# Kernel optimization log

Measured on AMD Instinct MI355X. Metric: run time of the kernel, lower is better.

Reference implementation:

```python
import jax, jax.numpy as jnp
import numpy as np

T, N, F_IN, H1, H2, F_OUT = 48, 4096, 64, 64, 32, 64

def setup_inputs() -> dict:
    key = jax.random.key(0)
    ks = jax.random.split(key, 14)
    sc = 0.05
    x = jax.random.normal(ks[0], (T, N, F_IN), jnp.float32)
    adj = jax.random.uniform(ks[1], (N, N), jnp.float32) / N  # roughly row-normalized dense adjacency
    fc_w = jax.random.normal(ks[2], (F_IN, H1), jnp.float32) * sc
    fc_b = jnp.zeros((H1,), jnp.float32)
    Wz = jax.random.normal(ks[3], (H1, F_OUT), jnp.float32) * sc
    Wr = jax.random.normal(ks[4], (H1, F_OUT), jnp.float32) * sc
    Wh = jax.random.normal(ks[5], (H1, F_OUT), jnp.float32) * sc
    Lz = jax.random.normal(ks[6], (2 * F_OUT, F_OUT), jnp.float32) * sc
    Lr = jax.random.normal(ks[7], (2 * F_OUT, F_OUT), jnp.float32) * sc
    Lh = jax.random.normal(ks[8], (2 * F_OUT, F_OUT), jnp.float32) * sc
    bz = jnp.zeros((F_OUT,), jnp.float32)
    br = jnp.zeros((F_OUT,), jnp.float32)
    bh = jnp.zeros((F_OUT,), jnp.float32)
    return {"x": x, "adj": adj, "fc_w": fc_w, "fc_b": fc_b,
            "Wz": Wz, "Wr": Wr, "Wh": Wh,
            "Lz": Lz, "Lr": Lr, "Lh": Lh,
            "bz": bz, "br": br, "bh": bh}

def reference(x, adj, fc_w, fc_b, Wz, Wr, Wh, Lz, Lr, Lh, bz, br, bh):
    # relu(fc(x)) followed by relu(unsqueeze) == single relu
    xh = jax.nn.relu(x @ fc_w + fc_b)          # [T, N, H1]
    h0 = jnp.zeros((N, F_OUT), x.dtype)

    def step(h, xi):
        # TGCN cell: dense graph conv A @ (X W) feeding GRU-style gates
        az = adj @ (xi @ Wz)                   # [N, F_OUT]
        ar = adj @ (xi @ Wr)
        ah = adj @ (xi @ Wh)
        z = jax.nn.sigmoid(jnp.concatenate([az, h], axis=-1) @ Lz + bz)
        r = jax.nn.sigmoid(jnp.concatenate([ar, h], axis=-1) @ Lr + br)
        h_tilde = jnp.tanh(jnp.concatenate([ah, h * r], axis=-1) @ Lh + bh)
        h_new = z * h + (1.0 - z) * h_tilde
        return h_new, None

    h, _ = jax.lax.scan(step, h0, xh)
    return h[None]                              # [1, N, F_OUT]
```

## Files before the change

kernel.cpp:

```cpp
#include <hip/hip_runtime.h>

typedef unsigned short u16;
typedef unsigned char u8;
typedef short s16x8 __attribute__((ext_vector_type(8)));
typedef unsigned short u16x4 __attribute__((ext_vector_type(4)));
typedef float f32x4 __attribute__((ext_vector_type(4)));
typedef int i32x4 __attribute__((ext_vector_type(4)));
typedef int i32x8 __attribute__((ext_vector_type(8)));

#define AS1 __attribute__((address_space(1)))
#define AS3 __attribute__((address_space(3)))

__device__ __forceinline__ void g2l16(const void* g, void* l) {
  __builtin_amdgcn_global_load_lds((const AS1 void*)g, (AS3 void*)l, 16, 0, 0);
}

__device__ __forceinline__ float b2f(u16 u) {
  union { unsigned int i; float f; } x; x.i = ((unsigned int)u) << 16; return x.f;
}
__device__ __forceinline__ u16 f2b(float f) {
  unsigned int u = __builtin_bit_cast(unsigned int, f);
  return (u16)((u + 0x7fffu + ((u >> 16) & 1u)) >> 16);
}
__device__ __forceinline__ u8 f2e4m3(float v) {
  int p = __builtin_amdgcn_cvt_pk_fp8_f32(v, 0.f, 0, false);
  return (u8)(p & 0xff);
}
__device__ __forceinline__ float sigm(float x) { return 1.f / (1.f + __expf(-x)); }
__device__ __forceinline__ float tanh_f(float x) { return 2.f / (1.f + __expf(-2.f * x)) - 1.f; }


__global__ __launch_bounds__(256) void kpre(
    const float* __restrict__ a, u8* __restrict__ ab,
    const float* __restrict__ fcw, const float* __restrict__ fcb,
    const float* __restrict__ x, u8* __restrict__ xht,
    const float* __restrict__ Wz, const float* __restrict__ Wr, const float* __restrict__ Wh,
    const float* __restrict__ Lz, const float* __restrict__ Lr, const float* __restrict__ Lh,
    u16* __restrict__ wct, u16* __restrict__ lbt) {
  int b = blockIdx.x, tid = threadIdx.x;
  if (b < 4096) {
    size_t idx = (size_t)b * 256 + tid;
    const float4* src = (const float4*)a;
    unsigned int* dst = (unsigned int*)ab;
#pragma unroll
    for (int k = 0; k < 4; ++k) {
      float4 v = src[idx + (size_t)k * 1048576];
      unsigned int p = __builtin_amdgcn_cvt_pk_fp8_f32(v.x * 4096.f, v.y * 4096.f, 0, false);
      p = __builtin_amdgcn_cvt_pk_fp8_f32(v.z * 4096.f, v.w * 4096.f, p, true);
      dst[idx + (size_t)k * 1048576] = p;
    }
    return;
  }
  if (b < 4144) {
    int idx = (b - 4096) * 256 + tid;
    int c_cat = idx >> 6, hh = idx & 63;
    int g = c_cat >> 6, c = c_cat & 63;
    const float* W = (g == 0) ? Wz : (g == 1) ? Wr : Wh;
    const float* L = (g == 0) ? Lz : (g == 1) ? Lr : Lh;
    float acc = 0.f;
    for (int m = 0; m < 64; ++m) acc += W[hh * 64 + m] * L[m * 64 + c];
    wct[c_cat * 64 + hh] = f2b(acc);
    return;
  }
  if (b < 4147) {
    int g = b - 4144;
    const float* L = (g == 0) ? Lz : (g == 1) ? Lr : Lh;
    for (int i = 0; i < 16; ++i) {
      int idx = tid * 16 + i; int c = idx >> 6, hh = idx & 63;
      lbt[g * 4096 + c * 64 + hh] = f2b(L[(64 + hh) * 64 + c]);
    }
    return;
  }
  int kb = b - 4147;
  int t = kb >> 5, n0 = (kb & 31) * 128;
  __shared__ __align__(16) u16 xs[128 * 72];
  __shared__ __align__(16) u16 fw[64 * 72];
  __shared__ __align__(16) u8 xh8[64 * 128];
  __shared__ float fb[64];
  int w = tid >> 6, l = tid & 63;
#pragma unroll
  for (int i = 0; i < 16; ++i) {
    int idx = tid + i * 256;
    int h = idx & 63, f = idx >> 6;
    fw[h * 72 + f] = f2b(fcw[f * 64 + h]);
  }
  const float4* xg = (const float4*)(x + ((size_t)t * 4096 + n0) * 64);
#pragma unroll
  for (int i = 0; i < 8; ++i) {
    int f = tid + i * 256;
    float4 v = xg[f];
    u16x4 p; p[0] = f2b(v.x); p[1] = f2b(v.y); p[2] = f2b(v.z); p[3] = f2b(v.w);
    *(u16x4*)&xs[(f >> 4) * 72 + (f & 15) * 4] = p;
  }
  if (tid < 64) fb[tid] = fcb[tid];
  __syncthreads();

  int lm = l & 15, q = l >> 4;
  f32x4 acc[4][2];
#pragma unroll
  for (int i = 0; i < 4; ++i)
#pragma unroll
    for (int j = 0; j < 2; ++j)
#pragma unroll
      for (int r = 0; r < 4; ++r) acc[i][j][r] = 0.f;
#pragma unroll
  for (int s = 0; s < 2; ++s) {
    s16x8 af[4], bf[2];
#pragma unroll
    for (int i = 0; i < 4; ++i) af[i] = *(const s16x8*)&fw[(16 * i + lm) * 72 + 32 * s + q * 8];
#pragma unroll
    for (int j = 0; j < 2; ++j) bf[j] = *(const s16x8*)&xs[(32 * w + 16 * j + lm) * 72 + 32 * s + q * 8];
#pragma unroll
    for (int i = 0; i < 4; ++i)
#pragma unroll
      for (int j = 0; j < 2; ++j)
        acc[i][j] = __builtin_amdgcn_mfma_f32_16x16x32_bf16(af[i], bf[j], acc[i][j], 0, 0, 0);
  }
#pragma unroll
  for (int i = 0; i < 4; ++i)
#pragma unroll
    for (int j = 0; j < 2; ++j) {
      int node = 32 * w + 16 * j + lm;
      int h0 = 16 * i + q * 4;
#pragma unroll
      for (int r = 0; r < 4; ++r) {
        float v = acc[i][j][r] + fb[h0 + r];
        xh8[(h0 + r) * 128 + node] = f2e4m3(v > 0.f ? v : 0.f);
      }
    }
  __syncthreads();
  {
    int h = tid >> 2, seg = tid & 3;
    u8* dst = xht + (size_t)(t * 64 + h) * 4096 + n0 + seg * 32;
    const u8* src = &xh8[h * 128 + seg * 32];
    *(i32x4*)dst = *(const i32x4*)src;
    *(i32x4*)(dst + 16) = *(const i32x4*)(src + 16);
  }
}

__global__ __launch_bounds__(256, 2) void k2(
    const u8* __restrict__ A, const u8* __restrict__ B, u16* __restrict__ M) {
  __shared__ __align__(16) u8 sh[49152];
  int tid = threadIdx.x, w = tid >> 6, l = tid & 63;
  int nt = blockIdx.x, mt = blockIdx.y;
  const u8* Ab = A + (size_t)mt * 128 * 4096;
  const u8* Bb = B + (size_t)nt * 192 * 4096;
  int lm = l & 15, q = l >> 4;
  int wm = w >> 1, wn = w & 1;
  int srow = l >> 3, scol = l & 7;
  f32x4 acc[4][6];
#pragma unroll
  for (int i = 0; i < 4; ++i)
#pragma unroll
    for (int j = 0; j < 6; ++j)
#pragma unroll
      for (int r = 0; r < 4; ++r) acc[i][j][r] = 0.f;

#define STAGE_B(bsel, kk)                                                     \
  do {                                                                        \
    _Pragma("unroll") for (int j = 0; j < 6; ++j) {                           \
      int r0 = 48 * w + 8 * j;                                                \
      int row = r0 + srow;                                                    \
      int c = (scol - row) & 7;                                               \
      g2l16(Bb + (size_t)row * 4096 + (kk) + c * 16,                          \
            sh + (bsel) * 24576 + r0 * 128);                                  \
    }                                                                         \
  } while (0)

  STAGE_B(0, 0);
  __syncthreads();

  for (int it = 0; it < 32; ++it) {
    int k0b = it * 128;
    int cur = it & 1;
    i32x8 a8[4];
#pragma unroll
    for (int i = 0; i < 4; ++i) {
      int ra = 64 * wm + 16 * i + lm;
      a8[i] = *(const i32x8*)(Ab + (size_t)ra * 4096 + k0b + q * 32);
    }
    if (it < 31) STAGE_B(cur ^ 1, k0b + 128);
    const u8* Bs = sh + cur * 24576;
#pragma unroll
    for (int j = 0; j < 6; ++j) {
      int rb = 96 * wn + 16 * j + lm;
      int q0 = (2 * q + rb) & 7, q1 = (2 * q + 1 + rb) & 7;
      i32x4 lo = *(const i32x4*)&Bs[rb * 128 + q0 * 16];
      i32x4 hi = *(const i32x4*)&Bs[rb * 128 + q1 * 16];
      i32x8 b8 = __builtin_shufflevector(lo, hi, 0, 1, 2, 3, 4, 5, 6, 7);
#pragma unroll
      for (int i = 0; i < 4; ++i)
        acc[i][j] = __builtin_amdgcn_mfma_scale_f32_16x16x128_f8f6f4(
            a8[i], b8, acc[i][j], 0, 0, 0, 127, 0, 127);
    }
    __syncthreads();
  }
#undef STAGE_B

  u16* tb = (u16*)sh;
  const float sc = 1.f / 4096.f;
#pragma unroll
  for (int p = 0; p < 2; ++p) {
    if (p) __syncthreads();
    if (wm == p) {
#pragma unroll
      for (int i = 0; i < 4; ++i)
#pragma unroll
        for (int j = 0; j < 6; ++j)
#pragma unroll
          for (int r = 0; r < 4; ++r)
            tb[(16 * i + 4 * q + r) * 200 + 96 * wn + 16 * j + lm] = f2b(acc[i][j][r] * sc);
    }
    __syncthreads();
    int row = tid >> 2, seg = tid & 3;
    u16* dst = M + (size_t)(mt * 128 + p * 64 + row) * 3072 + nt * 192 + seg * 48;
    const u16* src = &tb[row * 200 + seg * 48];
#pragma unroll
    for (int v = 0; v < 6; ++v)
      *(i32x4*)(dst + 8 * v) = *(const i32x4*)(src + 8 * v);
  }
}

__global__ __launch_bounds__(256) void k3(
    const u16* __restrict__ M, const u16* __restrict__ wct, const u16* __restrict__ lbt,
    const float* __restrict__ bz, const float* __restrict__ br, const float* __restrict__ bh,
    float* __restrict__ out) {
  __shared__ __align__(16) u16 hhi[16 * 72], hlo[16 * 72];
  __shared__ __align__(16) u16 rhi[16 * 72], rlo[16 * 72];
  int tid = threadIdx.x, w = tid >> 6, l = tid & 63;
  int nb0 = blockIdx.x * 16;
  int lm = l & 15, q = l >> 4;
  int cb = 16 * w + q * 4;
  s16x8 afw[3][2], afl[3][2];
#pragma unroll
  for (int g = 0; g < 3; ++g)
#pragma unroll
    for (int s = 0; s < 2; ++s) {
      afw[g][s] = *(const s16x8*)&wct[(size_t)(g * 64 + 16 * w + lm) * 64 + 32 * s + q * 8];
      afl[g][s] = *(const s16x8*)&lbt[(size_t)(g * 64 + 16 * w + lm) * 64 + 32 * s + q * 8];
    }
  for (int i = tid; i < 16 * 72; i += 256) { hhi[i] = 0; hlo[i] = 0; }
  f32x4 bzv, brv, bhv, hv;
#pragma unroll
  for (int r = 0; r < 4; ++r) {
    bzv[r] = bz[cb + r]; brv[r] = br[cb + r]; bhv[r] = bh[cb + r]; hv[r] = 0.f;
  }
  __syncthreads();

  const u16* Mrow = M + (size_t)(nb0 + lm) * 3072;
  s16x8 Mn[2];
  Mn[0] = *(const s16x8*)&Mrow[q * 8];
  Mn[1] = *(const s16x8*)&Mrow[32 + q * 8];

  for (int t = 0; t < 48; ++t) {
    s16x8 Mc[2] = {Mn[0], Mn[1]};
    if (t < 47) {
      Mn[0] = *(const s16x8*)&Mrow[(t + 1) * 64 + q * 8];
      Mn[1] = *(const s16x8*)&Mrow[(t + 1) * 64 + 32 + q * 8];
    }
    f32x4 uzw, uzh, urw, urh;
#pragma unroll
    for (int r = 0; r < 4; ++r) { uzw[r] = 0.f; uzh[r] = 0.f; urw[r] = 0.f; urh[r] = 0.f; }
#pragma unroll
    for (int s = 0; s < 2; ++s) {
      s16x8 hh = *(const s16x8*)&hhi[lm * 72 + 32 * s + q * 8];
      s16x8 hl = *(const s16x8*)&hlo[lm * 72 + 32 * s + q * 8];
      uzw = __builtin_amdgcn_mfma_f32_16x16x32_bf16(afw[0][s], Mc[s], uzw, 0, 0, 0);
      uzh = __builtin_amdgcn_mfma_f32_16x16x32_bf16(afl[0][s], hh, uzh, 0, 0, 0);
      uzh = __builtin_amdgcn_mfma_f32_16x16x32_bf16(afl[0][s], hl, uzh, 0, 0, 0);
      urw = __builtin_amdgcn_mfma_f32_16x16x32_bf16(afw[1][s], Mc[s], urw, 0, 0, 0);
      urh = __builtin_amdgcn_mfma_f32_16x16x32_bf16(afl[1][s], hh, urh, 0, 0, 0);
      urh = __builtin_amdgcn_mfma_f32_16x16x32_bf16(afl[1][s], hl, urh, 0, 0, 0);
    }
    f32x4 zv, rv;
#pragma unroll
    for (int r = 0; r < 4; ++r) {
      zv[r] = sigm(uzw[r] + uzh[r] + bzv[r]);
      rv[r] = sigm(urw[r] + urh[r] + brv[r]);
    }
    {
      u16x4 phi, plo;
#pragma unroll
      for (int r = 0; r < 4; ++r) {
        float p = hv[r] * rv[r];
        u16 hi = f2b(p); phi[r] = hi; plo[r] = f2b(p - b2f(hi));
      }
      *(u16x4*)&rhi[lm * 72 + cb] = phi;
      *(u16x4*)&rlo[lm * 72 + cb] = plo;
    }
    __syncthreads();
    f32x4 uhw, uhh;
#pragma unroll
    for (int r = 0; r < 4; ++r) { uhw[r] = 0.f; uhh[r] = 0.f; }
#pragma unroll
    for (int s = 0; s < 2; ++s) {
      s16x8 rh = *(const s16x8*)&rhi[lm * 72 + 32 * s + q * 8];
      s16x8 rl = *(const s16x8*)&rlo[lm * 72 + 32 * s + q * 8];
      uhw = __builtin_amdgcn_mfma_f32_16x16x32_bf16(afw[2][s], Mc[s], uhw, 0, 0, 0);
      uhh = __builtin_amdgcn_mfma_f32_16x16x32_bf16(afl[2][s], rh, uhh, 0, 0, 0);
      uhh = __builtin_amdgcn_mfma_f32_16x16x32_bf16(afl[2][s], rl, uhh, 0, 0, 0);
    }
    {
      u16x4 phi, plo;
#pragma unroll
      for (int r = 0; r < 4; ++r) {
        float th = tanh_f(uhw[r] + uhh[r] + bhv[r]);
        float hn = zv[r] * hv[r] + (1.f - zv[r]) * th;
        hv[r] = hn;
        u16 hi = f2b(hn); phi[r] = hi; plo[r] = f2b(hn - b2f(hi));
      }
      *(u16x4*)&hhi[lm * 72 + cb] = phi;
      *(u16x4*)&hlo[lm * 72 + cb] = plo;
    }
    __syncthreads();
  }
#pragma unroll
  for (int r = 0; r < 4; ++r)
    out[(size_t)(nb0 + lm) * 64 + cb + r] = hv[r];
}

extern "C" void kernel_launch(void* const* d_in, const int* in_sizes, int n_in,
                              void* d_out, int out_size, void* d_ws, size_t ws_size,
                              hipStream_t stream) {
  const float* x   = (const float*)d_in[0];
  const float* adj = (const float*)d_in[1];
  const float* fcw = (const float*)d_in[2];
  const float* fcb = (const float*)d_in[3];
  const float* Wz  = (const float*)d_in[4];
  const float* Wr  = (const float*)d_in[5];
  const float* Wh  = (const float*)d_in[6];
  const float* Lz  = (const float*)d_in[7];
  const float* Lr  = (const float*)d_in[8];
  const float* Lh  = (const float*)d_in[9];
  const float* bz  = (const float*)d_in[10];
  const float* br  = (const float*)d_in[11];
  const float* bh  = (const float*)d_in[12];
  char* ws = (char*)d_ws;
  u8*  xht  = (u8*)(ws);
  u8*  adj8 = (u8*)(ws + (size_t)12582912);
  u16* Mm   = (u16*)(ws + (size_t)29360128);
  u16* wct  = (u16*)(ws + (size_t)54525952);
  u16* lbt  = (u16*)(ws + (size_t)54550528);
  float* outp = (float*)d_out;

  hipLaunchKernelGGL(kpre, dim3(5683), dim3(256), 0, stream,
                     adj, adj8, fcw, fcb, x, xht, Wz, Wr, Wh, Lz, Lr, Lh, wct, lbt);
  hipLaunchKernelGGL(k2, dim3(16, 32), dim3(256), 0, stream, adj8, xht, Mm);
  hipLaunchKernelGGL(k3, dim3(256), dim3(256), 0, stream, Mm, wct, lbt, bz, br, bh, outp);
}
```

Baseline: 285.9 us.

## Stage A tiles through LDS alongside B in double-buffered k2 GEMM

The A operand of the fp8 MFMA GEMM was read straight from global memory into registers each iteration. It is now loaded asynchronously into LDS with the same swizzled global_load_lds scheme used for B, double-buffered, and read back from LDS with conflict-avoiding offsets. The prefetch of the next stage is also issued before the current compute. LDS per block grows from 48KB to 80KB and the occupancy hint of 2 blocks per CU is dropped, which may reduce concurrency.

Result: faster. 259.3 us (-9.3%).

```diff
diff --git a/kernel.cpp b/kernel.cpp
--- a/kernel.cpp
+++ b/kernel.cpp
@@ -138,9 +138,9 @@
   }
 }
 
-__global__ __launch_bounds__(256, 2) void k2(
+__global__ __launch_bounds__(256) void k2(
     const u8* __restrict__ A, const u8* __restrict__ B, u16* __restrict__ M) {
-  __shared__ __align__(16) u8 sh[49152];
+  __shared__ __align__(16) u8 sh[81920];
   int tid = threadIdx.x, w = tid >> 6, l = tid & 63;
   int nt = blockIdx.x, mt = blockIdx.y;
   const u8* Ab = A + (size_t)mt * 128 * 4096;
@@ -156,38 +156,49 @@
 #pragma unroll
       for (int r = 0; r < 4; ++r) acc[i][j][r] = 0.f;
 
-#define STAGE_B(bsel, kk)                                                     \
+#define STAGE(bsel, kk)                                                       \
   do {                                                                        \
-    _Pragma("unroll") for (int j = 0; j < 6; ++j) {                           \
+    u8* As_ = sh + (bsel) * 40960;                                            \
+    u8* Bs_ = As_ + 16384;                                                    \
+    _Pragma("unroll") for (int j = 0; j < 4; ++j) {      \
+      int r0 = 32 * w + 8 * j;                                                \
+      int row = r0 + srow;                                                    \
+      int c = (scol - row) & 7;                                               \
+      g2l16(Ab + (size_t)row * 4096 + (kk) + c * 16, As_ + r0 * 128);         \
+    }                                                                         \
+    _Pragma("unroll") for (int j = 0; j < 6; ++j) {      \
       int r0 = 48 * w + 8 * j;                                                \
       int row = r0 + srow;                                                    \
       int c = (scol - row) & 7;                                               \
-      g2l16(Bb + (size_t)row * 4096 + (kk) + c * 16,                          \
-            sh + (bsel) * 24576 + r0 * 128);                                  \
+      g2l16(Bb + (size_t)row * 4096 + (kk) + c * 16, Bs_ + r0 * 128);         \
     }                                                                         \
   } while (0)
 
-  STAGE_B(0, 0);
+  STAGE(0, 0);
   __syncthreads();
 
   for (int it = 0; it < 32; ++it) {
     int k0b = it * 128;
     int cur = it & 1;
+    if (it < 31) STAGE(cur ^ 1, k0b + 128);
+    const u8* As = sh + cur * 40960;
+    const u8* Bs = As + 16384;
     i32x8 a8[4];
 #pragma unroll
     for (int i = 0; i < 4; ++i) {
       int ra = 64 * wm + 16 * i + lm;
-      a8[i] = *(const i32x8*)(Ab + (size_t)ra * 4096 + k0b + q * 32);
-    }
-    if (it < 31) STAGE_B(cur ^ 1, k0b + 128);
-    const u8* Bs = sh + cur * 24576;
+      int p0 = (2 * q + ra) & 7, p1 = (2 * q + 1 + ra) & 7;
+      i32x4 lo = *(const i32x4*)&As[ra * 128 + p0 * 16];
+      i32x4 hi = *(const i32x4*)&As[ra * 128 + p1 * 16];
+      a8[i] = __builtin_shufflevector(lo, hi, 0, 1, 2, 3, 4, 5, 6, 7);
+    }
 #pragma unroll
     for (int j = 0; j < 6; ++j) {
       int rb = 96 * wn + 16 * j + lm;
       int q0 = (2 * q + rb) & 7, q1 = (2 * q + 1 + rb) & 7;
-      i32x4 lo = *(const i32x4*)&Bs[rb * 128 + q0 * 16];
-      i32x4 hi = *(const i32x4*)&Bs[rb * 128 + q1 * 16];
-      i32x8 b8 = __builtin_shufflevector(lo, hi, 0, 1, 2, 3, 4, 5, 6, 7);
+      i32x4 lo2 = *(const i32x4*)&Bs[rb * 128 + q0 * 16];
+      i32x4 hi2 = *(const i32x4*)&Bs[rb * 128 + q1 * 16];
+      i32x8 b8 = __builtin_shufflevector(lo2, hi2, 0, 1, 2, 3, 4, 5, 6, 7);
 #pragma unroll
       for (int i = 0; i < 4; ++i)
         acc[i][j] = __builtin_amdgcn_mfma_scale_f32_16x16x128_f8f6f4(
@@ -195,7 +206,7 @@
     }
     __syncthreads();
   }
-#undef STAGE_B
+#undef STAGE
 
   u16* tb = (u16*)sh;
   const float sc = 1.f / 4096.f;
```
